# Optimization experiments

Hardware: AMD Instinct MI355X
Metric: run time of the kernel (lower is better)

Reference implementation:

```python
import jax, jax.numpy as jnp
import numpy as np

POS_NUM = 60
TWO_PI = 2.0 * np.pi


def setup_inputs() -> dict:
    key = jax.random.key(0)
    k1, k2 = jax.random.split(key)
    B = 262144
    # [r1, r3, r4, r5, thc]; positive link lengths / angle in a realistic range
    pred_tensor = jax.random.uniform(k1, (B, 5), minval=0.1, maxval=2.0, dtype=jnp.float32)
    target_tensor = jax.random.normal(k2, (B, 2 * POS_NUM), dtype=jnp.float32)
    return {"pred_tensor": pred_tensor, "target_tensor": target_tensor}


def _compute_pos(pred, th2_min, th2_max, n):
    """Vectorized version of PosLoss.compute_pos.
    pred: [B,9] = [r1,r2,r3,r4,th1,r5,alpha,x0,y0]; th2_min/th2_max: [B].
    Returns interleaved coupler positions [B, 2n] = [x0,y0,x1,y1,...]."""
    dt = pred.dtype
    step = (th2_max - th2_min) / (n - 1)                     # [B]
    th2 = th2_min[:, None] + step[:, None] * jnp.arange(n, dtype=dt)  # [B,n]
    r1, r2, r3, r4 = pred[:, 0:1], pred[:, 1:2], pred[:, 2:3], pred[:, 3:4]
    th1, r5, al = pred[:, 4:5], pred[:, 5:6], pred[:, 6:7]
    x0, y0 = pred[:, 7:8], pred[:, 8:9]
    k1 = r1**2 + r2**2 + r3**2 - r4**2 - 2.0 * r1 * r2 * jnp.cos(th2 - th1)
    k2 = 2.0 * r1 * r3 * jnp.cos(th1) - 2.0 * r2 * r3 * jnp.cos(th2)
    k3 = 2.0 * r1 * r3 * jnp.sin(th1) - 2.0 * r2 * r3 * jnp.sin(th2)
    a = k1 + k2
    b = -2.0 * k3
    c = k1 - k2
    disc = b * b - 4.0 * a * c
    bad = disc < 0                                            # == isnan(sqrt(disc))
    D = jnp.sqrt(jnp.where(bad, 0.0, disc))
    th3 = 2.0 * jnp.arctan((-b + D) / (2.0 * a))
    p1x = jnp.where(bad, 0.0, r2 * jnp.cos(th2) + r5 * jnp.cos(al + th3) + x0)
    p1y = jnp.where(bad, 0.0, r2 * jnp.sin(th2) + r5 * jnp.sin(al + th3) + y0)
    return jnp.stack([p1x, p1y], axis=-1).reshape(pred.shape[0], 2 * n)


def reference(pred_tensor, target_tensor):
    n = POS_NUM
    dt = pred_tensor.dtype
    B = pred_tensor.shape[0]
    zeros = jnp.zeros((B,), dt)
    ones = jnp.ones((B,), dt)
    # pred9 = [r1, r2=1, r3, r4, th1=0, r5, alpha=thc, x0=0, y0=0]
    pred9 = jnp.stack([pred_tensor[:, 0], ones, pred_tensor[:, 1], pred_tensor[:, 2],
                       zeros, pred_tensor[:, 3], pred_tensor[:, 4], zeros, zeros], axis=1)
    L = pred9[:, :4]
    valid = 2.0 * jnp.max(L, axis=1) < jnp.sum(L, axis=1)
    c1 = (L[:, 0] + L[:, 1] - (L[:, 2] + L[:, 3])) > 0
    c2 = (jnp.abs(L[:, 0] - L[:, 1]) - jnp.abs(L[:, 2] - L[:, 3])) >= 0
    up = valid & c1 & c2
    low = valid & (~c1) & (~c2)
    bo = valid & c1 & (~c2)
    no = valid & (~c1) & c2
    denom = 2.0 * L[:, 0] * L[:, 1]
    arg_sum = (L[:, 0] ** 2 + L[:, 1] ** 2 - (L[:, 2] + L[:, 3]) ** 2) / denom
    arg_diff = (L[:, 0] ** 2 + L[:, 1] ** 2 - (L[:, 2] - L[:, 3]) ** 2) / denom
    acos_sum = jnp.arccos(jnp.where(up | bo, arg_sum, 0.0))
    acos_diff = jnp.arccos(jnp.where(low | bo, arg_diff, 0.0))
    th2_min = jnp.where(up, -acos_sum, jnp.where(low | bo, acos_diff, 0.0))
    th2_max = jnp.where(up | bo, acos_sum, jnp.where(low, TWO_PI - acos_diff, TWO_PI))
    # Sanitize rows that never contribute (invalid) so no NaN/Inf leaks in.
    safe_row = jnp.asarray([2.0, 1.0, 2.0, 2.0, 0.0, 1.0, 0.0, 0.0, 0.0], dt)
    pred_eff = jnp.where(valid[:, None], pred9, safe_row)
    th2_min = jnp.where(valid, th2_min, 0.0)
    th2_max = jnp.where(valid, th2_max, TWO_PI)
    pos = _compute_pos(pred_eff, th2_min, th2_max, n)         # [B, 2n]
    sq = (pos - target_tensor) ** 2

    def msum(m, x):
        return jnp.sum(jnp.where(m[:, None], x, 0.0))

    invalid_loss = msum(~valid, target_tensor ** 2)           # pos == 0 for invalid rows
    up_loss = msum(up, sq)
    low_loss = msum(low, sq)
    bo_loss = msum(bo, sq)
    no_loss = msum(no, sq)
    Nf = jnp.asarray(B, dt)
    return (invalid_loss / Nf, up_loss / Nf, low_loss / Nf, bo_loss / Nf, no_loss / Nf)
```

## Files before the change

kernel.cpp:

```cpp
#include <hip/hip_runtime.h>
#include <math.h>

#define CHUNK 32
#define NPOS 60
#define TWO_PI_F 6.283185307179586f
#define INV_TWO_PI_F 0.15915494309189535f
#define PI_F 3.14159265358979f

__device__ __forceinline__ float bcastf(float v, int l) {
    return __builtin_bit_cast(float, __builtin_amdgcn_readlane(__builtin_bit_cast(int, v), l));
}

__device__ __forceinline__ float acos_poly(float x) {
    const float ax = fabsf(x);
    const float s = __builtin_amdgcn_sqrtf(fmaxf(0.0f, 1.0f - ax));
    float p = fmaf(ax, -0.0187293f, 0.0742610f);
    p = fmaf(ax, p, -0.2121144f);
    p = fmaf(ax, p, 1.5707288f);
    const float r = s * p;
    return (x < 0.0f) ? (PI_F - r) : r;
}

__device__ __forceinline__ void hw_sincos_rev(float rev, float* s, float* c) {
    const float f = __builtin_amdgcn_fractf(rev);
    *s = __builtin_amdgcn_sinf(f);
    *c = __builtin_amdgcn_cosf(f);
}

__device__ __forceinline__ void row_acc(
    int rr, float txj, float tyj, float flane, bool inpos,
    float th2min_rev, float stp_rev, float ca5, float sa5,
    float P, float Q, float R, float S, float Bb, int cat,
    float& a0, float& a1, float& a2, float& a3, float& a4)
{
    const int catr    = __builtin_amdgcn_readlane(cat, rr);
    const float rev0  = bcastf(th2min_rev, rr);
    const float stp_r = bcastf(stp_rev, rr);
    const float ca5_r = bcastf(ca5, rr);
    const float sa5_r = bcastf(sa5, rr);
    const float P_r   = bcastf(P, rr);
    const float Q_r   = bcastf(Q, rr);
    const float R_r   = bcastf(R, rr);
    const float S_r   = bcastf(S, rr);
    const float Bb_r  = bcastf(Bb, rr);

    const float rev = fmaf(stp_r, flane, rev0);
    float sth, cth;
    hw_sincos_rev(rev, &sth, &cth);
    const float a  = fmaf(-Q_r, cth, P_r);
    const float cc = fmaf(-S_r, cth, R_r);
    const float b  = Bb_r * sth;
    const float t  = a * cc;
    const float bb = b * b;
    const float disc = fmaf(-4.0f, t, bb);
    const bool bad = disc < 0.0f;
    const float D = __builtin_amdgcn_sqrtf(fmaxf(disc, 0.0f));
    const float w = D - b;
    const float s = a + a;
    const float s2 = s * s, w2 = w * w;
    const float rden = __builtin_amdgcn_rcpf(s2 + w2);
    const float c3 = (s2 - w2) * rden;
    const float sw = s * w;
    const float s3 = (sw + sw) * rden;
    float px = fmaf(ca5_r, c3, fmaf(-sa5_r, s3, cth));
    float py = fmaf(sa5_r, c3, fmaf(ca5_r, s3, sth));
    px = bad ? 0.0f : px;
    py = bad ? 0.0f : py;
    const float dx = px - txj, dy = py - tyj;
    float ch = fmaf(dx, dx, dy * dy);
    ch = inpos ? ch : 0.0f;
    const float c0 = fmaf(txj, txj, tyj * tyj);
    a0 += (catr == 0) ? c0 : 0.0f;
    a1 += (catr == 1) ? ch : 0.0f;
    a2 += (catr == 2) ? ch : 0.0f;
    a3 += (catr == 3) ? ch : 0.0f;
    a4 += (catr == 4) ? ch : 0.0f;
}

__device__ __forceinline__ float2 ldt(const float* __restrict__ target,
                                      int base, int rr, int lane, bool inpos) {
    float2 tv = make_float2(0.0f, 0.0f);
    if (inpos) {
        tv = *reinterpret_cast<const float2*>(
            target + (size_t)(base + rr) * (size_t)(2 * NPOS) + 2 * lane);
    }
    return tv;
}

#define LOADB(Pfx, r0)                                                                     \
    do {                                                                                   \
        float2 _v;                                                                         \
        _v = ldt(target, base, (r0) + 0, lane, inpos); Pfx##x0 = _v.x; Pfx##y0 = _v.y;     \
        _v = ldt(target, base, (r0) + 1, lane, inpos); Pfx##x1 = _v.x; Pfx##y1 = _v.y;     \
        _v = ldt(target, base, (r0) + 2, lane, inpos); Pfx##x2 = _v.x; Pfx##y2 = _v.y;     \
        _v = ldt(target, base, (r0) + 3, lane, inpos); Pfx##x3 = _v.x; Pfx##y3 = _v.y;     \
        _v = ldt(target, base, (r0) + 4, lane, inpos); Pfx##x4 = _v.x; Pfx##y4 = _v.y;     \
        _v = ldt(target, base, (r0) + 5, lane, inpos); Pfx##x5 = _v.x; Pfx##y5 = _v.y;     \
        _v = ldt(target, base, (r0) + 6, lane, inpos); Pfx##x6 = _v.x; Pfx##y6 = _v.y;     \
        _v = ldt(target, base, (r0) + 7, lane, inpos); Pfx##x7 = _v.x; Pfx##y7 = _v.y;     \
    } while (0)

#define ROWA(Pfx, rr, sx, sy)                                                              \
    row_acc((rr), Pfx##sx, Pfx##sy, flane, inpos, th2min_rev, stp_rev, ca5, sa5,           \
            Pc, Qc, Rc, Sc, Bb, cat, a0, a1, a2, a3, a4)

#define COMPUTEB(Pfx, r0)                                                                  \
    do {                                                                                   \
        ROWA(Pfx, (r0) + 0, x0, y0);                                                       \
        ROWA(Pfx, (r0) + 1, x1, y1);                                                       \
        ROWA(Pfx, (r0) + 2, x2, y2);                                                       \
        ROWA(Pfx, (r0) + 3, x3, y3);                                                       \
        ROWA(Pfx, (r0) + 4, x4, y4);                                                       \
        ROWA(Pfx, (r0) + 5, x5, y5);                                                       \
        ROWA(Pfx, (r0) + 6, x6, y6);                                                       \
        ROWA(Pfx, (r0) + 7, x7, y7);                                                       \
    } while (0)

__global__ __launch_bounds__(256, 4) void posloss_main(
    const float* __restrict__ pred, const float* __restrict__ target,
    float* __restrict__ partials, int B, int nchunks)
{
    const int tid  = threadIdx.x;
    const int lane = tid & 63;
    const int wv   = tid >> 6;
    const int wid  = (blockIdx.x * blockDim.x + tid) >> 6;
    const bool inpos = lane < NPOS;
    const float flane = (float)lane;

    float a0 = 0.f, a1 = 0.f, a2 = 0.f, a3 = 0.f, a4 = 0.f;

    if (wid < nchunks) {
        const int base = wid * CHUNK;
        const int rmax = (B - base) < CHUNK ? (B - base) : CHUNK;

        const int prow = base + (lane & 31);
        float r1 = 2.f, r3 = 2.f, r4 = 2.f, r5 = 1.f, al = 0.f;
        if (prow < B) {
            const float* pp = pred + (size_t)prow * 5;
            r1 = pp[0]; r3 = pp[1]; r4 = pp[2]; r5 = pp[3]; al = pp[4];
        }

        const float sumL = ((r1 + 1.0f) + r3) + r4;
        const float maxL = fmaxf(fmaxf(r1, 1.0f), fmaxf(r3, r4));
        const bool valid = (2.0f * maxL) < sumL;
        const bool c1 = ((r1 + 1.0f) - (r3 + r4)) > 0.0f;
        const bool c2 = (fabsf(r1 - 1.0f) - fabsf(r3 - r4)) >= 0.0f;
        const bool up = valid && c1 && c2;
        const bool lo = valid && (!c1) && (!c2);
        const bool bo = valid && c1 && (!c2);
        const float rdenom = __builtin_amdgcn_rcpf(2.0f * r1);
        const float s34 = r3 + r4, d34 = r3 - r4;
        const float r1sq1 = fmaf(r1, r1, 1.0f);
        float argS = (r1sq1 - s34 * s34) * rdenom;
        float argD = (r1sq1 - d34 * d34) * rdenom;
        argS = (up || bo) ? argS : 0.0f;
        argD = (lo || bo) ? argD : 0.0f;
        argS = fminf(1.0f, fmaxf(-1.0f, argS));
        argD = fminf(1.0f, fmaxf(-1.0f, argD));
        const float acS = acos_poly(argS);
        const float acD = acos_poly(argD);
        float th2min = up ? (-acS) : ((lo || bo) ? acD : 0.0f);
        float th2max = (up || bo) ? acS : (lo ? (TWO_PI_F - acD) : TWO_PI_F);
        if (!valid) { th2min = 0.0f; th2max = TWO_PI_F; }
        const float stp_rev    = (th2max - th2min) * (INV_TWO_PI_F / 59.0f);
        const float th2min_rev = th2min * INV_TWO_PI_F;
        const int cat = (!valid) ? 0 : (up ? 1 : (lo ? 2 : (bo ? 3 : 4)));
        float sal, cal;
        hw_sincos_rev(al * INV_TWO_PI_F, &sal, &cal);
        const float ca5 = r5 * cal, sa5 = r5 * sal;
        const float K1c = fmaf(r3, r3, r1sq1) - r4 * r4;
        const float K1m = 2.0f * r1;
        const float A2  = (2.0f * r1) * r3;
        const float B2  = 2.0f * r3;
        const float Pc = K1c + A2;
        const float Qc = K1m + B2;
        const float Rc = K1c - A2;
        const float Sc = K1m - B2;
        const float Bb = 2.0f * B2;

        if (rmax == CHUNK) {
            float Ax0,Ay0,Ax1,Ay1,Ax2,Ay2,Ax3,Ay3,Ax4,Ay4,Ax5,Ay5,Ax6,Ay6,Ax7,Ay7;
            float Bx0,By0,Bx1,By1,Bx2,By2,Bx3,By3,Bx4,By4,Bx5,By5,Bx6,By6,Bx7,By7;
            LOADB(A, 0);
            LOADB(B, 8);
            COMPUTEB(A, 0);
            LOADB(A, 16);
            COMPUTEB(B, 8);
            LOADB(B, 24);
            COMPUTEB(A, 16);
            COMPUTEB(B, 24);
        } else {
            for (int rr = 0; rr < rmax; ++rr) {
                const float2 tv = ldt(target, base, rr, lane, inpos);
                row_acc(rr, tv.x, tv.y, flane, inpos, th2min_rev, stp_rev, ca5, sa5,
                        Pc, Qc, Rc, Sc, Bb, cat, a0, a1, a2, a3, a4);
            }
        }
    }

    for (int off = 32; off; off >>= 1) {
        a0 += __shfl_xor(a0, off);
        a1 += __shfl_xor(a1, off);
        a2 += __shfl_xor(a2, off);
        a3 += __shfl_xor(a3, off);
        a4 += __shfl_xor(a4, off);
    }
    __shared__ float red[4][5];
    if (lane == 0) {
        red[wv][0] = a0; red[wv][1] = a1; red[wv][2] = a2; red[wv][3] = a3; red[wv][4] = a4;
    }
    __syncthreads();
    if (tid < 5) {
        const float s = ((red[0][tid] + red[1][tid]) + red[2][tid]) + red[3][tid];
        partials[(size_t)tid * gridDim.x + blockIdx.x] = s;
    }
}

__global__ void posloss_reduce(const float* __restrict__ partials, float* __restrict__ out,
                               int nblocks, int B)
{
    const int w = threadIdx.x >> 6, lane = threadIdx.x & 63;
    if (w >= 5) return;
    double s0 = 0.0, s1 = 0.0, s2 = 0.0, s3 = 0.0;
    const float* p = partials + (size_t)w * nblocks;
    for (int k = lane; k + 192 < nblocks; k += 256) {
        s0 += (double)p[k];
        s1 += (double)p[k + 64];
        s2 += (double)p[k + 128];
        s3 += (double)p[k + 192];
    }
    double s = (s0 + s1) + (s2 + s3);
    for (int off = 32; off; off >>= 1) s += __shfl_down(s, off);
    if (lane == 0) out[w] = (float)(s / (double)B);
}

extern "C" void kernel_launch(void* const* d_in, const int* in_sizes, int n_in,
                              void* d_out, int out_size, void* d_ws, size_t ws_size,
                              hipStream_t stream) {
    (void)n_in; (void)out_size; (void)ws_size;
    const float* pred   = (const float*)d_in[0];
    const float* target = (const float*)d_in[1];
    float* out = (float*)d_out;
    float* partials = (float*)d_ws;
    const int B = in_sizes[0] / 5;
    const int nchunks = (B + CHUNK - 1) / CHUNK;
    const int nblocks = 2048;
    posloss_main<<<nblocks, 256, 0, stream>>>(pred, target, partials, B, nchunks);
    posloss_reduce<<<1, 320, 0, stream>>>(partials, out, nblocks, B);
}
```

Measured before the change: 45.40 us.

## Skip invalid-row math, shrink load batches, raise occupancy, replace reduce kernel with atomics

For rows in the invalid category, each row step now does only the target-squared accumulation and returns before the trigonometric and quadratic math. Category accumulation becomes a branch chain instead of five selects. The double-buffered target loads drop from eight rows to four per buffer to cut register pressure, and the launch bounds ask for eight waves per SIMD. The separate reduction kernel is replaced by a memset plus per-block float atomicAdd into the output, which removes a launch but makes the summation order nondeterministic and less precise than the earlier double-precision reduction.

```diff
diff --git a/kernel.cpp b/kernel.cpp
--- a/kernel.cpp
+++ b/kernel.cpp
@@ -33,7 +33,11 @@
     float P, float Q, float R, float S, float Bb, int cat,
     float& a0, float& a1, float& a2, float& a3, float& a4)
 {
-    const int catr    = __builtin_amdgcn_readlane(cat, rr);
+    const int catr = __builtin_amdgcn_readlane(cat, rr);
+    if (catr == 0) {
+        a0 += fmaf(txj, txj, tyj * tyj);
+        return;
+    }
     const float rev0  = bcastf(th2min_rev, rr);
     const float stp_r = bcastf(stp_rev, rr);
     const float ca5_r = bcastf(ca5, rr);
@@ -50,9 +54,7 @@
     const float a  = fmaf(-Q_r, cth, P_r);
     const float cc = fmaf(-S_r, cth, R_r);
     const float b  = Bb_r * sth;
-    const float t  = a * cc;
-    const float bb = b * b;
-    const float disc = fmaf(-4.0f, t, bb);
+    const float disc = fmaf(b, b, -4.0f * (a * cc));
     const bool bad = disc < 0.0f;
     const float D = __builtin_amdgcn_sqrtf(fmaxf(disc, 0.0f));
     const float w = D - b;
@@ -69,12 +71,10 @@
     const float dx = px - txj, dy = py - tyj;
     float ch = fmaf(dx, dx, dy * dy);
     ch = inpos ? ch : 0.0f;
-    const float c0 = fmaf(txj, txj, tyj * tyj);
-    a0 += (catr == 0) ? c0 : 0.0f;
-    a1 += (catr == 1) ? ch : 0.0f;
-    a2 += (catr == 2) ? ch : 0.0f;
-    a3 += (catr == 3) ? ch : 0.0f;
-    a4 += (catr == 4) ? ch : 0.0f;
+    if      (catr == 1) a1 += ch;
+    else if (catr == 2) a2 += ch;
+    else if (catr == 3) a3 += ch;
+    else                a4 += ch;
 }
 
 __device__ __forceinline__ float2 ldt(const float* __restrict__ target,
@@ -87,38 +87,30 @@
     return tv;
 }
 
-#define LOADB(Pfx, r0)                                                                     \
+#define LOADB4(Pfx, r0)                                                                    \
     do {                                                                                   \
         float2 _v;                                                                         \
         _v = ldt(target, base, (r0) + 0, lane, inpos); Pfx##x0 = _v.x; Pfx##y0 = _v.y;     \
         _v = ldt(target, base, (r0) + 1, lane, inpos); Pfx##x1 = _v.x; Pfx##y1 = _v.y;     \
         _v = ldt(target, base, (r0) + 2, lane, inpos); Pfx##x2 = _v.x; Pfx##y2 = _v.y;     \
         _v = ldt(target, base, (r0) + 3, lane, inpos); Pfx##x3 = _v.x; Pfx##y3 = _v.y;     \
-        _v = ldt(target, base, (r0) + 4, lane, inpos); Pfx##x4 = _v.x; Pfx##y4 = _v.y;     \
-        _v = ldt(target, base, (r0) + 5, lane, inpos); Pfx##x5 = _v.x; Pfx##y5 = _v.y;     \
-        _v = ldt(target, base, (r0) + 6, lane, inpos); Pfx##x6 = _v.x; Pfx##y6 = _v.y;     \
-        _v = ldt(target, base, (r0) + 7, lane, inpos); Pfx##x7 = _v.x; Pfx##y7 = _v.y;     \
     } while (0)
 
 #define ROWA(Pfx, rr, sx, sy)                                                              \
     row_acc((rr), Pfx##sx, Pfx##sy, flane, inpos, th2min_rev, stp_rev, ca5, sa5,           \
             Pc, Qc, Rc, Sc, Bb, cat, a0, a1, a2, a3, a4)
 
-#define COMPUTEB(Pfx, r0)                                                                  \
+#define COMPUTEB4(Pfx, r0)                                                                 \
     do {                                                                                   \
         ROWA(Pfx, (r0) + 0, x0, y0);                                                       \
         ROWA(Pfx, (r0) + 1, x1, y1);                                                       \
         ROWA(Pfx, (r0) + 2, x2, y2);                                                       \
         ROWA(Pfx, (r0) + 3, x3, y3);                                                       \
-        ROWA(Pfx, (r0) + 4, x4, y4);                                                       \
-        ROWA(Pfx, (r0) + 5, x5, y5);                                                       \
-        ROWA(Pfx, (r0) + 6, x6, y6);                                                       \
-        ROWA(Pfx, (r0) + 7, x7, y7);                                                       \
     } while (0)
 
-__global__ __launch_bounds__(256, 4) void posloss_main(
+__global__ __launch_bounds__(256, 8) void posloss_main(
     const float* __restrict__ pred, const float* __restrict__ target,
-    float* __restrict__ partials, int B, int nchunks)
+    float* __restrict__ out, int B, int nchunks)
 {
     const int tid  = threadIdx.x;
     const int lane = tid & 63;
@@ -179,16 +171,18 @@
         const float Bb = 2.0f * B2;
 
         if (rmax == CHUNK) {
-            float Ax0,Ay0,Ax1,Ay1,Ax2,Ay2,Ax3,Ay3,Ax4,Ay4,Ax5,Ay5,Ax6,Ay6,Ax7,Ay7;
-            float Bx0,By0,Bx1,By1,Bx2,By2,Bx3,By3,Bx4,By4,Bx5,By5,Bx6,By6,Bx7,By7;
-            LOADB(A, 0);
-            LOADB(B, 8);
-            COMPUTEB(A, 0);
-            LOADB(A, 16);
-            COMPUTEB(B, 8);
-            LOADB(B, 24);
-            COMPUTEB(A, 16);
-            COMPUTEB(B, 24);
+            float Ax0,Ay0,Ax1,Ay1,Ax2,Ay2,Ax3,Ay3;
+            float Bx0,By0,Bx1,By1,Bx2,By2,Bx3,By3;
+            LOADB4(A, 0);
+            LOADB4(B, 4);
+            COMPUTEB4(A, 0);  LOADB4(A, 8);
+            COMPUTEB4(B, 4);  LOADB4(B, 12);
+            COMPUTEB4(A, 8);  LOADB4(A, 16);
+            COMPUTEB4(B, 12); LOADB4(B, 20);
+            COMPUTEB4(A, 16); LOADB4(A, 24);
+            COMPUTEB4(B, 20); LOADB4(B, 28);
+            COMPUTEB4(A, 24);
+            COMPUTEB4(B, 28);
         } else {
             for (int rr = 0; rr < rmax; ++rr) {
                 const float2 tv = ldt(target, base, rr, lane, inpos);
@@ -212,39 +206,21 @@
     __syncthreads();
     if (tid < 5) {
         const float s = ((red[0][tid] + red[1][tid]) + red[2][tid]) + red[3][tid];
-        partials[(size_t)tid * gridDim.x + blockIdx.x] = s;
-    }
-}
-
-__global__ void posloss_reduce(const float* __restrict__ partials, float* __restrict__ out,
-                               int nblocks, int B)
-{
-    const int w = threadIdx.x >> 6, lane = threadIdx.x & 63;
-    if (w >= 5) return;
-    double s0 = 0.0, s1 = 0.0, s2 = 0.0, s3 = 0.0;
-    const float* p = partials + (size_t)w * nblocks;
-    for (int k = lane; k + 192 < nblocks; k += 256) {
-        s0 += (double)p[k];
-        s1 += (double)p[k + 64];
-        s2 += (double)p[k + 128];
-        s3 += (double)p[k + 192];
-    }
-    double s = (s0 + s1) + (s2 + s3);
-    for (int off = 32; off; off >>= 1) s += __shfl_down(s, off);
-    if (lane == 0) out[w] = (float)(s / (double)B);
+        const float invB = 1.0f / (float)B;
+        atomicAdd(&out[tid], s * invB);
+    }
 }
 
 extern "C" void kernel_launch(void* const* d_in, const int* in_sizes, int n_in,
                               void* d_out, int out_size, void* d_ws, size_t ws_size,
                               hipStream_t stream) {
-    (void)n_in; (void)out_size; (void)ws_size;
+    (void)n_in; (void)out_size; (void)d_ws; (void)ws_size;
     const float* pred   = (const float*)d_in[0];
     const float* target = (const float*)d_in[1];
     float* out = (float*)d_out;
-    float* partials = (float*)d_ws;
     const int B = in_sizes[0] / 5;
     const int nchunks = (B + CHUNK - 1) / CHUNK;
-    const int nblocks = 2048;
-    posloss_main<<<nblocks, 256, 0, stream>>>(pred, target, partials, B, nchunks);
-    posloss_reduce<<<1, 320, 0, stream>>>(partials, out, nblocks, B);
-}
+    const int nblocks = (nchunks + 3) / 4;
+    hipMemsetAsync(out, 0, 5 * sizeof(float), stream);
+    posloss_main<<<nblocks, 256, 0, stream>>>(pred, target, out, B, nchunks);
+}
```

New measurement: 61.62 us. 1.36x slower.
